# Performance work log

Hardware: AMD Instinct MI355X
Metric: run time of the kernel (lower is better)

Reference implementation:

```python
import jax, jax.numpy as jnp
import numpy as np

B, N = 4096, 512


def setup_inputs() -> dict:
    key = jax.random.key(0)
    ks = jax.random.split(key, 8)
    waypoints = jax.random.normal(ks[0], (B, N, 2), dtype=jnp.float32)
    # learned params: scalar smooth_weight + curvature_net MLP (4->64->32->1)
    smooth_weight = jnp.float32(0.3)
    W1 = jax.random.normal(ks[1], (4, 64), dtype=jnp.float32) * 0.5
    b1 = jnp.zeros((64,), dtype=jnp.float32)
    W2 = jax.random.normal(ks[2], (64, 32), dtype=jnp.float32) * 0.125
    b2 = jnp.zeros((32,), dtype=jnp.float32)
    W3 = jax.random.normal(ks[3], (32, 1), dtype=jnp.float32) * 0.18
    b3 = jnp.zeros((1,), dtype=jnp.float32)
    return {"waypoints": waypoints, "smooth_weight": smooth_weight,
            "W1": W1, "b1": b1, "W2": W2, "b2": b2, "W3": W3, "b3": b3}


def _forward(waypoints, smooth_weight, W1, b1, W2, b2, W3, b3):
    Bq, Nq, _ = waypoints.shape
    # finite differences
    d1 = waypoints[:, 1:] - waypoints[:, :-1]          # (B, N-1, 2)
    d2 = d1[:, 1:] - d1[:, :-1]                        # (B, N-2, 2)
    d1 = jnp.concatenate([d1, d1[:, -1:]], axis=1)     # (B, N, 2)
    z = jnp.zeros((Bq, 1, 2), dtype=waypoints.dtype)
    d2 = jnp.concatenate([z, d2, z], axis=1)           # (B, N, 2)
    feats = jnp.concatenate([d1, d2], axis=-1)         # (B, N, 4)
    # curvature MLP -> sigmoid weight in (0,1)
    h = jax.nn.relu(jnp.einsum('bnf,fh->bnh', feats, W1) + b1)
    h = jax.nn.relu(jnp.einsum('bnh,hk->bnk', h, W2) + b2)
    cw = jax.nn.sigmoid(jnp.einsum('bnk,ko->bno', h, W3) + b3)  # (B, N, 1)
    sw = jax.nn.sigmoid(smooth_weight)
    w = sw * (1.0 - cw[..., 0])                        # (B, N)
    # linear recurrence: y_i = w_i * y_{i-1} + (1-w_i) * x_i, y_0 = x_0
    a = jnp.swapaxes(w[:, 1:], 0, 1)                   # (N-1, B)
    x = jnp.swapaxes(waypoints[:, 1:], 0, 1)           # (N-1, B, 2)

    def step(carry, inp):
        a_i, x_i = inp
        y = a_i[:, None] * carry + (1.0 - a_i)[:, None] * x_i
        return y, y

    _, ys = jax.lax.scan(step, waypoints[:, 0], (a, x))
    smoothed = jnp.concatenate([waypoints[:, :1], jnp.swapaxes(ys, 0, 1)], axis=1)
    # endpoints pinned to original (start already equals input)
    smoothed = smoothed.at[:, -1].set(waypoints[:, -1])
    return smoothed


def reference(waypoints, smooth_weight, W1, b1, W2, b2, W3, b3):
    return _forward(waypoints, smooth_weight, W1, b1, W2, b2, W3, b3)
```

## Files before the change

kernel.cpp:

```cpp
#include <hip/hip_runtime.h>
#include <math.h>

#define NPT 512
#define BROWS 4096
#define TAB_U4 10

typedef _Float16 half8  __attribute__((ext_vector_type(8)));
typedef _Float16 h2     __attribute__((ext_vector_type(2)));
typedef float    f32x16 __attribute__((ext_vector_type(16)));
typedef unsigned int u32x4 __attribute__((ext_vector_type(4)));

__device__ __forceinline__ float sigmoidf_fast(float x) {
    return 1.0f / (1.0f + __expf(-x));
}

__device__ __forceinline__ h2 pkrtz(float a, float b) {
    return __builtin_bit_cast(h2, __builtin_amdgcn_cvt_pkrtz(a, b));
}

#if __has_builtin(__builtin_amdgcn_fdot2)
__device__ __forceinline__ float fdot2(h2 a, h2 b, float c) {
    return __builtin_amdgcn_fdot2(__builtin_bit_cast(__fp16 __attribute__((ext_vector_type(2))), a),
                                  __builtin_bit_cast(__fp16 __attribute__((ext_vector_type(2))), b),
                                  c, false);
}
#else
__device__ __forceinline__ float fdot2(h2 a, h2 b, float c) {
    c = fmaf((float)a[0], (float)b[0], c);
    c = fmaf((float)a[1], (float)b[1], c);
    return c;
}
#endif

union H8 { half8 v; h2 p[4]; unsigned int w[4]; };

__device__ __forceinline__ f32x16 mfma32(half8 a, half8 b, f32x16 c) {
    return __builtin_amdgcn_mfma_f32_32x32x16_f16(a, b, c, 0, 0, 0);
}

__device__ __forceinline__ void pl32swap(unsigned &a, unsigned &b) {
    asm volatile("v_permlane32_swap_b32 %0, %1" : "+v"(a), "+v"(b));
}

__device__ __forceinline__ half8 makeB2(unsigned p0, unsigned p1,
                                        unsigned p2, unsigned p3) {
    pl32swap(p0, p2);
    pl32swap(p1, p3);
    H8 B; B.w[0] = p0; B.w[1] = p1; B.w[2] = p2; B.w[3] = p3;
    return B.v;
}

__global__ __launch_bounds__(64) void setup_kernel(
    const float* __restrict__ W1, const float* __restrict__ b1,
    const float* __restrict__ W2, const float* __restrict__ b2,
    const float* __restrict__ W3, u32x4* __restrict__ tab)
{
    const int lane = threadIdx.x & 63;
    const int c    = lane & 31;
    const int hi   = lane >> 5;

    #pragma unroll
    for (int t = 0; t < 2; ++t) {
        H8 a;
        a.w[0] = 0u; a.w[1] = 0u; a.w[2] = 0u; a.w[3] = 0u;
        if (hi == 0) {
            const int ch = t * 32 + c;
            h2 v0; v0[0] = (_Float16)W1[0 * 64 + ch]; v0[1] = (_Float16)W1[1 * 64 + ch];
            h2 v1; v1[0] = (_Float16)W1[2 * 64 + ch]; v1[1] = (_Float16)W1[3 * 64 + ch];
            h2 v2; v2[0] = (_Float16)b1[ch];          v2[1] = (_Float16)0.f;
            a.p[0] = v0; a.p[1] = v1; a.p[2] = v2;
        }
        u32x4 o; o[0] = a.w[0]; o[1] = a.w[1]; o[2] = a.w[2]; o[3] = a.w[3];
        tab[t * 64 + lane] = o;
    }

    #pragma unroll
    for (int s = 0; s < 4; ++s) {
        H8 a;
        #pragma unroll
        for (int jj = 0; jj < 4; ++jj) {
            const int k = s * 16 + hi * 8 + 2 * jj;
            h2 v; v[0] = (_Float16)W2[k * 32 + c]; v[1] = (_Float16)W2[(k + 1) * 32 + c];
            a.p[jj] = v;
        }
        u32x4 o; o[0] = a.w[0]; o[1] = a.w[1]; o[2] = a.w[2]; o[3] = a.w[3];
        tab[(2 + s) * 64 + lane] = o;
    }

    unsigned bw[8], ww[8];
    #pragma unroll
    for (int rr = 0; rr < 8; ++rr) {
        const int q   = 2 * rr;
        const int row = (q & 3) + 8 * (q >> 2) + 4 * hi;
        h2 bv; bv[0] = (_Float16)b2[row]; bv[1] = (_Float16)b2[row + 1];
        h2 wv; wv[0] = (_Float16)W3[row]; wv[1] = (_Float16)W3[row + 1];
        bw[rr] = __builtin_bit_cast(unsigned, bv);
        ww[rr] = __builtin_bit_cast(unsigned, wv);
    }
    {
        u32x4 o0, o1, o2, o3;
        #pragma unroll
        for (int e = 0; e < 4; ++e) {
            o0[e] = bw[e]; o1[e] = bw[4 + e];
            o2[e] = ww[e]; o3[e] = ww[4 + e];
        }
        tab[6 * 64 + lane] = o0;
        tab[7 * 64 + lane] = o1;
        tab[8 * 64 + lane] = o2;
        tab[9 * 64 + lane] = o3;
    }
}

__global__ __launch_bounds__(256, 5) void wps_kernel(
    const float* __restrict__ wp,
    const float* __restrict__ sww,
    const float* __restrict__ b3,
    const u32x4* __restrict__ tab,
    float* __restrict__ out)
{
    __shared__ float sLg[2][NPT];
    __shared__ float2 sY[2];

    const int t    = threadIdx.x;
    const int lane = t & 63;
    const int wv   = t >> 6;
    const int row0 = blockIdx.x * 2;
    const int c    = lane & 31;

    half8 A1t[2];
    #pragma unroll
    for (int i = 0; i < 2; ++i) {
        u32x4 v = tab[i * 64 + lane];
        H8 a; a.w[0] = v[0]; a.w[1] = v[1]; a.w[2] = v[2]; a.w[3] = v[3];
        A1t[i] = a.v;
    }
    half8 A2s[4];
    #pragma unroll
    for (int i = 0; i < 4; ++i) {
        u32x4 v = tab[(2 + i) * 64 + lane];
        H8 a; a.w[0] = v[0]; a.w[1] = v[1]; a.w[2] = v[2]; a.w[3] = v[3];
        A2s[i] = a.v;
    }
    h2 b2p[8], w3p[8];
    {
        u32x4 v0 = tab[6 * 64 + lane];
        u32x4 v1 = tab[7 * 64 + lane];
        u32x4 v2 = tab[8 * 64 + lane];
        u32x4 v3 = tab[9 * 64 + lane];
        #pragma unroll
        for (int e = 0; e < 4; ++e) {
            b2p[e]     = __builtin_bit_cast(h2, (unsigned)v0[e]);
            b2p[4 + e] = __builtin_bit_cast(h2, (unsigned)v1[e]);
            w3p[e]     = __builtin_bit_cast(h2, (unsigned)v2[e]);
            w3p[4 + e] = __builtin_bit_cast(h2, (unsigned)v3[e]);
        }
    }

    h2 zeroh; zeroh[0] = (_Float16)0.f; zeroh[1] = (_Float16)0.f;
    const f32x16 zero16 = {0.f,0.f,0.f,0.f,0.f,0.f,0.f,0.f,
                           0.f,0.f,0.f,0.f,0.f,0.f,0.f,0.f};

    const int seg = wv * 128;

    #pragma unroll
    for (int r = 0; r < 2; ++r) {
        const float2* P = (const float2*)(wp + (size_t)(row0 + r) * NPT * 2);

        #pragma unroll
        for (int s2 = 0; s2 < 2; ++s2) {
            const int base = seg + s2 * 64;
            const int g    = base + lane;

            float2 p  = P[g];
            float2 pm = P[(g > 0) ? g - 1 : 0];
            float2 pp = P[(g < NPT - 1) ? g + 1 : NPT - 1];
            float d1x, d1y;
            if (g < NPT - 1) { d1x = pp.x - p.x; d1y = pp.y - p.y; }
            else             { d1x = p.x - pm.x; d1y = p.y - pm.y; }
            float d2x = 0.f, d2y = 0.f;
            if (g >= 1 && g <= NPT - 2) {
                d2x = pp.x - 2.f * p.x + pm.x;
                d2y = pp.y - 2.f * p.y + pm.y;
            }
            const int u01 = __builtin_bit_cast(int, pkrtz(d1x, d1y));
            const int u23 = __builtin_bit_cast(int, pkrtz(d2x, d2y));

            #pragma unroll
            for (int T = 0; T < 2; ++T) {
                const unsigned r01 = (unsigned)__shfl(u01, T * 32 + c);
                const unsigned r23 = (unsigned)__shfl(u23, T * 32 + c);
                H8 B1;
                B1.w[0] = r01; B1.w[1] = r23;
                B1.w[2] = 0x00003C00u; B1.w[3] = 0u;

                f32x16 pre0 = mfma32(A1t[0], B1.v, zero16);
                f32x16 pre1 = mfma32(A1t[1], B1.v, zero16);

                unsigned pw0[8], pw1[8];
                #pragma unroll
                for (int rr = 0; rr < 8; ++rr) {
                    pw0[rr] = __builtin_bit_cast(unsigned,
                        __builtin_elementwise_max(pkrtz(pre0[2*rr], pre0[2*rr+1]), zeroh));
                    pw1[rr] = __builtin_bit_cast(unsigned,
                        __builtin_elementwise_max(pkrtz(pre1[2*rr], pre1[2*rr+1]), zeroh));
                }

                f32x16 acc = zero16;
                acc = mfma32(A2s[0], makeB2(pw0[0], pw0[1], pw0[2], pw0[3]), acc);
                acc = mfma32(A2s[1], makeB2(pw0[4], pw0[5], pw0[6], pw0[7]), acc);
                acc = mfma32(A2s[2], makeB2(pw1[0], pw1[1], pw1[2], pw1[3]), acc);
                acc = mfma32(A2s[3], makeB2(pw1[4], pw1[5], pw1[6], pw1[7]), acc);

                float v = 0.f;
                #pragma unroll
                for (int rr = 0; rr < 8; ++rr) {
                    h2 tt = pkrtz(acc[2*rr], acc[2*rr+1]);
                    tt = tt + b2p[rr];
                    tt = __builtin_elementwise_max(tt, zeroh);
                    v = fdot2(tt, w3p[rr], v);
                }
                v += __shfl_xor(v, 32);
                if (lane < 32) sLg[r][base + T * 32 + lane] = v;
            }
        }
    }

    __syncthreads();

    {
        const int rloc = wv >> 1;
        const int half = wv & 1;
        const int row  = row0 + rloc;
        const float2* P = (const float2*)(wp + (size_t)row * NPT * 2);
        const float bias3 = b3[0];
        const float swv   = sigmoidf_fast(sww[0]);

        const int base = half * 256 + lane * 4;
        float wr[4];
        *reinterpret_cast<float4*>(&wr[0]) =
            *reinterpret_cast<const float4*>(&sLg[rloc][base]);

        const float4* P4 = (const float4*)P;
        float2 pts[4];
        #pragma unroll
        for (int s = 0; s < 2; ++s) {
            float4 v = P4[base / 2 + s];
            pts[2 * s].x     = v.x; pts[2 * s].y     = v.y;
            pts[2 * s + 1].x = v.z; pts[2 * s + 1].y = v.w;
        }

        float a4[4], cx4[4], cy4[4];
        float A = 1.f, Cx = 0.f, Cy = 0.f;
        #pragma unroll
        for (int i = 0; i < 4; ++i) {
            const int g = base + i;
            float a = (g == 0) ? 0.f
                               : swv * (1.f - sigmoidf_fast(wr[i] + bias3));
            float cx = (1.f - a) * pts[i].x;
            float cy = (1.f - a) * pts[i].y;
            a4[i] = a; cx4[i] = cx; cy4[i] = cy;
            Cx = fmaf(a, Cx, cx);
            Cy = fmaf(a, Cy, cy);
            A *= a;
        }
        #pragma unroll
        for (int d = 1; d < 64; d <<= 1) {
            float Ap  = __shfl_up(A, d);
            float Cpx = __shfl_up(Cx, d);
            float Cpy = __shfl_up(Cy, d);
            if (lane >= d) {
                Cx = fmaf(A, Cpx, Cx);
                Cy = fmaf(A, Cpy, Cy);
                A *= Ap;
            }
        }
        float Aex  = __shfl_up(A, 1);
        float Cxex = __shfl_up(Cx, 1);
        float Cyex = __shfl_up(Cy, 1);

        float4* orow = (float4*)(out + (size_t)row * NPT * 2);

        if (half == 0) {
            float yx = (lane == 0) ? 0.f : Cxex;
            float yy = (lane == 0) ? 0.f : Cyex;
            float ox[4], oy[4];
            #pragma unroll
            for (int i = 0; i < 4; ++i) {
                yx = fmaf(a4[i], yx, cx4[i]);
                yy = fmaf(a4[i], yy, cy4[i]);
                ox[i] = yx; oy[i] = yy;
            }
            orow[base / 2]     = make_float4(ox[0], oy[0], ox[1], oy[1]);
            orow[base / 2 + 1] = make_float4(ox[2], oy[2], ox[3], oy[3]);
            if (lane == 63) { sY[rloc].x = yx; sY[rloc].y = yy; }
        }

        __syncthreads();

        if (half == 1) {
            const float2 y255 = sY[rloc];
            float yx = (lane == 0) ? y255.x : fmaf(Aex, y255.x, Cxex);
            float yy = (lane == 0) ? y255.y : fmaf(Aex, y255.y, Cyex);
            float ox[4], oy[4];
            #pragma unroll
            for (int i = 0; i < 4; ++i) {
                yx = fmaf(a4[i], yx, cx4[i]);
                yy = fmaf(a4[i], yy, cy4[i]);
                ox[i] = yx; oy[i] = yy;
            }
            if (lane == 63) {
                float2 pe = P[NPT - 1];
                ox[3] = pe.x; oy[3] = pe.y;
            }
            orow[base / 2]     = make_float4(ox[0], oy[0], ox[1], oy[1]);
            orow[base / 2 + 1] = make_float4(ox[2], oy[2], ox[3], oy[3]);
        }
    }
}

extern "C" void kernel_launch(void* const* d_in, const int* in_sizes, int n_in,
                              void* d_out, int out_size, void* d_ws, size_t ws_size,
                              hipStream_t stream) {
    const float* wp  = (const float*)d_in[0];
    const float* sww = (const float*)d_in[1];
    const float* W1  = (const float*)d_in[2];
    const float* b1  = (const float*)d_in[3];
    const float* W2  = (const float*)d_in[4];
    const float* b2  = (const float*)d_in[5];
    const float* W3  = (const float*)d_in[6];
    const float* b3  = (const float*)d_in[7];
    float* out = (float*)d_out;
    u32x4* tab = (u32x4*)d_ws;

    setup_kernel<<<1, 64, 0, stream>>>(W1, b1, W2, b2, W3, tab);
    wps_kernel<<<BROWS / 2, 256, 0, stream>>>(wp, sww, b3, tab, out);
}
```

Before: 31.47 us.

## Fuse weight-packing setup into main kernel and split MFMA accumulator chain

```diff
diff --git a/kernel.cpp b/kernel.cpp
--- a/kernel.cpp
+++ b/kernel.cpp
@@ -3,12 +3,10 @@
 
 #define NPT 512
 #define BROWS 4096
-#define TAB_U4 10
 
 typedef _Float16 half8  __attribute__((ext_vector_type(8)));
 typedef _Float16 h2     __attribute__((ext_vector_type(2)));
 typedef float    f32x16 __attribute__((ext_vector_type(16)));
-typedef unsigned int u32x4 __attribute__((ext_vector_type(4)));
 
 __device__ __forceinline__ float sigmoidf_fast(float x) {
     return 1.0f / (1.0f + __expf(-x));
@@ -50,72 +48,15 @@
     return B.v;
 }
 
-__global__ __launch_bounds__(64) void setup_kernel(
-    const float* __restrict__ W1, const float* __restrict__ b1,
-    const float* __restrict__ W2, const float* __restrict__ b2,
-    const float* __restrict__ W3, u32x4* __restrict__ tab)
-{
-    const int lane = threadIdx.x & 63;
-    const int c    = lane & 31;
-    const int hi   = lane >> 5;
-
-    #pragma unroll
-    for (int t = 0; t < 2; ++t) {
-        H8 a;
-        a.w[0] = 0u; a.w[1] = 0u; a.w[2] = 0u; a.w[3] = 0u;
-        if (hi == 0) {
-            const int ch = t * 32 + c;
-            h2 v0; v0[0] = (_Float16)W1[0 * 64 + ch]; v0[1] = (_Float16)W1[1 * 64 + ch];
-            h2 v1; v1[0] = (_Float16)W1[2 * 64 + ch]; v1[1] = (_Float16)W1[3 * 64 + ch];
-            h2 v2; v2[0] = (_Float16)b1[ch];          v2[1] = (_Float16)0.f;
-            a.p[0] = v0; a.p[1] = v1; a.p[2] = v2;
-        }
-        u32x4 o; o[0] = a.w[0]; o[1] = a.w[1]; o[2] = a.w[2]; o[3] = a.w[3];
-        tab[t * 64 + lane] = o;
-    }
-
-    #pragma unroll
-    for (int s = 0; s < 4; ++s) {
-        H8 a;
-        #pragma unroll
-        for (int jj = 0; jj < 4; ++jj) {
-            const int k = s * 16 + hi * 8 + 2 * jj;
-            h2 v; v[0] = (_Float16)W2[k * 32 + c]; v[1] = (_Float16)W2[(k + 1) * 32 + c];
-            a.p[jj] = v;
-        }
-        u32x4 o; o[0] = a.w[0]; o[1] = a.w[1]; o[2] = a.w[2]; o[3] = a.w[3];
-        tab[(2 + s) * 64 + lane] = o;
-    }
-
-    unsigned bw[8], ww[8];
-    #pragma unroll
-    for (int rr = 0; rr < 8; ++rr) {
-        const int q   = 2 * rr;
-        const int row = (q & 3) + 8 * (q >> 2) + 4 * hi;
-        h2 bv; bv[0] = (_Float16)b2[row]; bv[1] = (_Float16)b2[row + 1];
-        h2 wv; wv[0] = (_Float16)W3[row]; wv[1] = (_Float16)W3[row + 1];
-        bw[rr] = __builtin_bit_cast(unsigned, bv);
-        ww[rr] = __builtin_bit_cast(unsigned, wv);
-    }
-    {
-        u32x4 o0, o1, o2, o3;
-        #pragma unroll
-        for (int e = 0; e < 4; ++e) {
-            o0[e] = bw[e]; o1[e] = bw[4 + e];
-            o2[e] = ww[e]; o3[e] = ww[4 + e];
-        }
-        tab[6 * 64 + lane] = o0;
-        tab[7 * 64 + lane] = o1;
-        tab[8 * 64 + lane] = o2;
-        tab[9 * 64 + lane] = o3;
-    }
-}
-
-__global__ __launch_bounds__(256, 5) void wps_kernel(
+__global__ __launch_bounds__(256, 4) void wps_kernel(
     const float* __restrict__ wp,
     const float* __restrict__ sww,
+    const float* __restrict__ W1,
+    const float* __restrict__ b1,
+    const float* __restrict__ W2,
+    const float* __restrict__ b2,
+    const float* __restrict__ W3,
     const float* __restrict__ b3,
-    const u32x4* __restrict__ tab,
     float* __restrict__ out)
 {
     __shared__ float sLg[2][NPT];
@@ -126,34 +67,43 @@
     const int wv   = t >> 6;
     const int row0 = blockIdx.x * 2;
     const int c    = lane & 31;
+    const int hi   = lane >> 5;
 
     half8 A1t[2];
     #pragma unroll
-    for (int i = 0; i < 2; ++i) {
-        u32x4 v = tab[i * 64 + lane];
-        H8 a; a.w[0] = v[0]; a.w[1] = v[1]; a.w[2] = v[2]; a.w[3] = v[3];
-        A1t[i] = a.v;
+    for (int tt = 0; tt < 2; ++tt) {
+        H8 a;
+        a.w[0] = 0u; a.w[1] = 0u; a.w[2] = 0u; a.w[3] = 0u;
+        if (hi == 0) {
+            const int ch = tt * 32 + c;
+            h2 v0; v0[0] = (_Float16)W1[0 * 64 + ch]; v0[1] = (_Float16)W1[1 * 64 + ch];
+            h2 v1; v1[0] = (_Float16)W1[2 * 64 + ch]; v1[1] = (_Float16)W1[3 * 64 + ch];
+            h2 v2; v2[0] = (_Float16)b1[ch];          v2[1] = (_Float16)0.f;
+            a.p[0] = v0; a.p[1] = v1; a.p[2] = v2;
+        }
+        A1t[tt] = a.v;
     }
     half8 A2s[4];
     #pragma unroll
-    for (int i = 0; i < 4; ++i) {
-        u32x4 v = tab[(2 + i) * 64 + lane];
-        H8 a; a.w[0] = v[0]; a.w[1] = v[1]; a.w[2] = v[2]; a.w[3] = v[3];
-        A2s[i] = a.v;
+    for (int s = 0; s < 4; ++s) {
+        H8 a;
+        #pragma unroll
+        for (int jj = 0; jj < 4; ++jj) {
+            const int k = s * 16 + hi * 8 + 2 * jj;
+            h2 v; v[0] = (_Float16)W2[k * 32 + c]; v[1] = (_Float16)W2[(k + 1) * 32 + c];
+            a.p[jj] = v;
+        }
+        A2s[s] = a.v;
     }
     h2 b2p[8], w3p[8];
-    {
-        u32x4 v0 = tab[6 * 64 + lane];
-        u32x4 v1 = tab[7 * 64 + lane];
-        u32x4 v2 = tab[8 * 64 + lane];
-        u32x4 v3 = tab[9 * 64 + lane];
-        #pragma unroll
-        for (int e = 0; e < 4; ++e) {
-            b2p[e]     = __builtin_bit_cast(h2, (unsigned)v0[e]);
-            b2p[4 + e] = __builtin_bit_cast(h2, (unsigned)v1[e]);
-            w3p[e]     = __builtin_bit_cast(h2, (unsigned)v2[e]);
-            w3p[4 + e] = __builtin_bit_cast(h2, (unsigned)v3[e]);
-        }
+    #pragma unroll
+    for (int rr = 0; rr < 8; ++rr) {
+        const int q   = 2 * rr;
+        const int row = (q & 3) + 8 * (q >> 2) + 4 * hi;
+        h2 bv; bv[0] = (_Float16)b2[row]; bv[1] = (_Float16)b2[row + 1];
+        h2 wv2; wv2[0] = (_Float16)W3[row]; wv2[1] = (_Float16)W3[row + 1];
+        b2p[rr] = bv;
+        w3p[rr] = wv2;
     }
 
     h2 zeroh; zeroh[0] = (_Float16)0.f; zeroh[1] = (_Float16)0.f;
@@ -205,19 +155,21 @@
                         __builtin_elementwise_max(pkrtz(pre1[2*rr], pre1[2*rr+1]), zeroh));
                 }
 
-                f32x16 acc = zero16;
-                acc = mfma32(A2s[0], makeB2(pw0[0], pw0[1], pw0[2], pw0[3]), acc);
-                acc = mfma32(A2s[1], makeB2(pw0[4], pw0[5], pw0[6], pw0[7]), acc);
-                acc = mfma32(A2s[2], makeB2(pw1[0], pw1[1], pw1[2], pw1[3]), acc);
-                acc = mfma32(A2s[3], makeB2(pw1[4], pw1[5], pw1[6], pw1[7]), acc);
+                f32x16 accA = zero16;
+                f32x16 accB = zero16;
+                accA = mfma32(A2s[0], makeB2(pw0[0], pw0[1], pw0[2], pw0[3]), accA);
+                accB = mfma32(A2s[1], makeB2(pw0[4], pw0[5], pw0[6], pw0[7]), accB);
+                accA = mfma32(A2s[2], makeB2(pw1[0], pw1[1], pw1[2], pw1[3]), accA);
+                accB = mfma32(A2s[3], makeB2(pw1[4], pw1[5], pw1[6], pw1[7]), accB);
 
                 float v = 0.f;
                 #pragma unroll
                 for (int rr = 0; rr < 8; ++rr) {
-                    h2 tt = pkrtz(acc[2*rr], acc[2*rr+1]);
-                    tt = tt + b2p[rr];
-                    tt = __builtin_elementwise_max(tt, zeroh);
-                    v = fdot2(tt, w3p[rr], v);
+                    h2 tt2 = pkrtz(accA[2*rr] + accB[2*rr],
+                                   accA[2*rr+1] + accB[2*rr+1]);
+                    tt2 = tt2 + b2p[rr];
+                    tt2 = __builtin_elementwise_max(tt2, zeroh);
+                    v = fdot2(tt2, w3p[rr], v);
                 }
                 v += __shfl_xor(v, 32);
                 if (lane < 32) sLg[r][base + T * 32 + lane] = v;
@@ -330,8 +282,6 @@
     const float* W3  = (const float*)d_in[6];
     const float* b3  = (const float*)d_in[7];
     float* out = (float*)d_out;
-    u32x4* tab = (u32x4*)d_ws;
-
-    setup_kernel<<<1, 64, 0, stream>>>(W1, b1, W2, b2, W3, tab);
-    wps_kernel<<<BROWS / 2, 256, 0, stream>>>(wp, sww, b3, tab, out);
-}
+
+    wps_kernel<<<BROWS / 2, 256, 0, stream>>>(wp, sww, W1, b1, W2, b2, W3, b3, out);
+}
```

After: 27.61 us. -12.3%, faster.
